# Kernel tuning notes

Hardware: AMD Instinct MI355X
Metric: run time of the kernel (lower is better)

Reference implementation:

```python
import jax, jax.numpy as jnp
import numpy as np

B, T, EMB, H = 8, 1024, 128, 8


def setup_inputs() -> dict:
    key = jax.random.key(0)
    ks = jax.random.split(key, 7)
    s = 0.02
    return {
        "x": jax.random.normal(ks[0], (B, T, EMB), dtype=jnp.float32),
        "mask": jax.random.randint(ks[1], (1, T, T), 0, 2, dtype=jnp.int32),
        "Wk": (jax.random.normal(ks[2], (EMB * H, EMB), dtype=jnp.float32) * s),
        "Wq": (jax.random.normal(ks[3], (EMB * H, EMB), dtype=jnp.float32) * s),
        "Wv": (jax.random.normal(ks[4], (EMB * H, EMB), dtype=jnp.float32) * s),
        "Wu": (jax.random.normal(ks[5], (EMB, EMB * H), dtype=jnp.float32) * s),
        "bu": (jax.random.normal(ks[6], (EMB,), dtype=jnp.float32) * s),
    }


def reference(x, mask, Wk, Wq, Wv, Wu, bu):
    b, t, e = x.shape  # e == emb; per-head dim also == emb in this module
    h = Wk.shape[0] // e
    # projections: (b,t,e) @ (e, h*e) -> (b,t,h,e) -> (b,h,t,e)
    q = (x @ Wq.T).reshape(b, t, h, e).transpose(0, 2, 1, 3)
    k = (x @ Wk.T).reshape(b, t, h, e).transpose(0, 2, 1, 3)
    v = (x @ Wv.T).reshape(b, t, h, e).transpose(0, 2, 1, 3)
    scale = e ** 0.25  # torch scales q and k each by e**(1/4)
    dot = jnp.einsum('bhqe,bhke->bhqk', q / scale, k / scale)
    # causal mask: strictly-upper triangle (offset=1) set to -inf FIRST
    causal = jnp.triu(jnp.ones((t, t), dtype=bool), k=1)
    dot = jnp.where(causal, -jnp.inf, dot)
    # padding mask: where mask==0 set to -1e9 (overwrites -inf where overlapping)
    dot = jnp.where(mask[:, None] == 0, jnp.float32(-1e9), dot)
    attn = jax.nn.softmax(dot, axis=-1)
    out = jnp.einsum('bhqk,bhke->bhqe', attn, v)
    out = out.transpose(0, 2, 1, 3).reshape(b, t, h * e)
    return out @ Wu.T + bu
```

## Files before the change

kernel.cpp:

```cpp
#include <hip/hip_runtime.h>

#define Bn 8
#define Hn 8
#define Tn 1024
#define Dn 128

typedef __attribute__((ext_vector_type(8))) short bf16x8;
typedef __attribute__((ext_vector_type(4))) float f32x4;

typedef __attribute__((address_space(3))) unsigned int lds_as_t;
typedef __attribute__((address_space(1))) const unsigned int glb_as_t;

static __device__ __forceinline__ void gload_lds16(const unsigned short* g, unsigned short* l) {
    __builtin_amdgcn_global_load_lds((glb_as_t*)g, (lds_as_t*)l, 16, 0, 0);
}
static __device__ __forceinline__ void gload_lds16b(const char* g, char* l) {
    __builtin_amdgcn_global_load_lds((glb_as_t*)g, (lds_as_t*)l, 16, 0, 0);
}

static __device__ __forceinline__ unsigned short f2bf(float f) {
    union { float f; unsigned int u; } v; v.f = f;
    unsigned int u = v.u;
    return (unsigned short)((u + 0x7FFFu + ((u >> 16) & 1u)) >> 16);
}
static __device__ __forceinline__ int pack_bf16_trunc(float lo, float hi) {
    union { float f; unsigned int u; } a, b;
    a.f = lo; b.f = hi;
    return (int)__builtin_amdgcn_perm(b.u, a.u, 0x07060302u);
}

__global__ __launch_bounds__(256, 2) void qkv_kernel(
    const float* __restrict__ x,  const float* __restrict__ Wq,
    const float* __restrict__ Wk, const float* __restrict__ Wv,
    const float* __restrict__ Wu, const int* __restrict__ mask,
    const float* __restrict__ bu, float* __restrict__ out,
    unsigned short* __restrict__ wuF, unsigned long long* __restrict__ mbits,
    char* __restrict__ Q, char* __restrict__ K, unsigned short* __restrict__ Vt)
{
    const int bx = blockIdx.x, by = blockIdx.y;
    const int tid  = threadIdx.x;
    const int wave = tid >> 6;
    const int lane = tid & 63;
    const int l16  = lane & 15;
    const int quad = lane >> 4;
    const int wm = wave & 1, wn = wave >> 1;
    const int which = by >> 3;
    const int h_ = by & 7;
    const int bid = h_ * 64 + bx;

    __shared__ __align__(16) unsigned short As[128 * 128];
    __shared__ __align__(16) unsigned short Bs[128 * 128];

    if (which == 0) {
        int base = (bid * 4 + wave) * 8;
#pragma unroll
        for (int i = 0; i < 8; i++) {
            int widx = base + i;
            int row = widx >> 4, kt = widx & 15;
            int v = mask[row * Tn + kt * 64 + lane];
            unsigned long long b = __ballot(v != 0);
            if (lane == 0) mbits[kt * Tn + row] = b;
        }
    } else if (which == 1) {
        if (tid < 32) {
            int id = bid * 32 + tid;
            int lane_ = id & 63;
            int fid = id >> 6;
            int nt = fid & 7, ks = (fid >> 3) & 3, h = fid >> 5;
            int row = nt * 16 + (lane_ & 15);
            int col = h * 128 + ks * 32 + (lane_ >> 4) * 8;
            const float* src = Wu + (size_t)row * 1024 + col;
            float4 f0 = *(const float4*)(src);
            float4 f1 = *(const float4*)(src + 4);
            unsigned short o[8];
            o[0] = f2bf(f0.x); o[1] = f2bf(f0.y); o[2] = f2bf(f0.z); o[3] = f2bf(f0.w);
            o[4] = f2bf(f1.x); o[5] = f2bf(f1.y); o[6] = f2bf(f1.z); o[7] = f2bf(f1.w);
            *(ushort4*)(wuF + (size_t)id * 8)     = *(ushort4*)&o[0];
            *(ushort4*)(wuF + (size_t)id * 8 + 4) = *(ushort4*)&o[4];
        }
    } else {
        int f4 = bid * 512 + tid * 2;
#pragma unroll
        for (int i = 0; i < 2; i++)
            ((float4*)out)[f4 + i] = ((const float4*)bu)[(f4 + i) & 31];
    }

    const float* wsel = (which == 0) ? Wq : (which == 1) ? Wk : Wv;
    const float* Asrc = x + (size_t)(bx * 128) * 128;
    const float* Bsrc = wsel + (size_t)(h_ * 128) * 128;

#pragma unroll
    for (int it = 0; it < 16; it++) {
        int idx = it * 1024 + tid * 4;
        int row = idx >> 7, col = idx & 127;
        int dst = row * 128 + ((((col >> 3) ^ (row & 15)) << 3) | (col & 7));
        float4 fa = *(const float4*)(Asrc + idx);
        ushort4 oa;
        oa.x = f2bf(fa.x); oa.y = f2bf(fa.y); oa.z = f2bf(fa.z); oa.w = f2bf(fa.w);
        *(ushort4*)(&As[dst]) = oa;
        float4 fb = *(const float4*)(Bsrc + idx);
        ushort4 ob;
        ob.x = f2bf(fb.x); ob.y = f2bf(fb.y); ob.z = f2bf(fb.z); ob.w = f2bf(fb.w);
        *(ushort4*)(&Bs[dst]) = ob;
    }
    __syncthreads();

    bf16x8 a[4][4];
#pragma unroll
    for (int mt = 0; mt < 4; mt++) {
        int row = wm * 64 + mt * 16 + l16;
#pragma unroll
        for (int ks = 0; ks < 4; ks++)
            a[mt][ks] = *(const bf16x8*)(&As[row * 128 + (((ks * 4 + quad) ^ (row & 15)) << 3)]);
    }

    f32x4 acc[4][4];
#pragma unroll
    for (int nt = 0; nt < 4; nt++) {
        int row = wn * 64 + nt * 16 + l16;
        bf16x8 b4[4];
#pragma unroll
        for (int ks = 0; ks < 4; ks++)
            b4[ks] = *(const bf16x8*)(&Bs[row * 128 + (((ks * 4 + quad) ^ (row & 15)) << 3)]);
#pragma unroll
        for (int mt = 0; mt < 4; mt++) {
            f32x4 c = {0.f, 0.f, 0.f, 0.f};
#pragma unroll
            for (int ks = 0; ks < 4; ks++)
                c = __builtin_amdgcn_mfma_f32_16x16x32_bf16(a[mt][ks], b4[ks], c, 0, 0, 0);
            acc[mt][nt] = c;
        }
    }

    const int b_ = bx >> 3;
    if (which < 2) {
        __syncthreads();
        char* escr = (char*)As;
#pragma unroll
        for (int mt = 0; mt < 4; mt++) {
#pragma unroll
            for (int nt = 0; nt < 4; nt++) {
                int w = __builtin_amdgcn_cvt_pk_fp8_f32(acc[mt][nt][0], acc[mt][nt][1], 0, false);
                w = __builtin_amdgcn_cvt_pk_fp8_f32(acc[mt][nt][2], acc[mt][nt][3], w, true);
                int col = wn * 64 + nt * 16 + l16;
#pragma unroll
                for (int r = 0; r < 4; r++)
                    escr[(wm * 64 + mt * 16 + quad * 4 + r) * 144 + col] = (char)(w >> (8 * r));
            }
        }
        __syncthreads();
        int row = tid >> 1;
        int t_in = (bx & 7) * 128 + row;
        char* dst = (which == 0) ? Q : K;
        size_t rowbase = ((size_t)((b_ * Hn + h_) * Tn + t_in)) * 128;
#pragma unroll
        for (int i = 0; i < 4; i++) {
            int c = (tid & 1) * 4 + i;
            int4 v = *(const int4*)(escr + row * 144 + c * 16);
            int cc = (which == 1) ? (c ^ (row & 7)) : c;
            *(int4*)(dst + rowbase + cc * 16) = v;
        }
    } else {
#pragma unroll
        for (int mt = 0; mt < 4; mt++) {
            int m_base = bx * 128 + wm * 64 + mt * 16 + quad * 4;
            int t0 = m_base & 1023;
#pragma unroll
            for (int nt = 0; nt < 4; nt++) {
                int e_ = wn * 64 + nt * 16 + l16;
                int kt_ = t0 >> 6, tc0 = t0 & 63;
                size_t off = ((((size_t)(b_ * Hn + h_) * 16 + kt_) * 128 + e_) << 6)
                           + ((((tc0 >> 3) ^ (e_ & 7)) << 3) | (tc0 & 7));
                ushort4 v4;
                v4.x = f2bf(acc[mt][nt][0]); v4.y = f2bf(acc[mt][nt][1]);
                v4.z = f2bf(acc[mt][nt][2]); v4.w = f2bf(acc[mt][nt][3]);
                *(ushort4*)(Vt + off) = v4;
            }
        }
    }
}

__global__ __launch_bounds__(256, 2) void attn_kernel(
    const char* __restrict__ Q,
    const char* __restrict__ K,
    const unsigned short* __restrict__ Vt,
    const unsigned long long* __restrict__ mbits,
    const unsigned short* __restrict__ wuF,
    float* __restrict__ out)
{
    const int id   = blockIdx.x;
    const int bh   = id & 63;
    const int t_   = id >> 6;
    const int qb   = (t_ < 4) ? t_ : 11 - t_;
    const int wave = threadIdx.x >> 6;
    const int lane = threadIdx.x & 63;
    const int l16  = lane & 15;
    const int quad = lane >> 4;

    __shared__ __align__(16) char kbuf[2][64 * 128];
    __shared__ __align__(16) unsigned short vbuf[2][128 * 64];

    const char* Qb = Q  + (size_t)bh * Tn * Dn;
    const char* Kb = K  + (size_t)bh * Tn * Dn;
    const unsigned short* Vb = Vt + (size_t)bh * (16 * 128 * 64);

    const int blkkt = 2 * qb + 1;
    const int q0w   = qb * 128 + wave * 32;
    const int q0s[2] = { q0w, q0w + 16 };
    const int wkmax = (q0w + 31) >> 6;

    long qf[2][4];
#pragma unroll
    for (int st = 0; st < 2; st++)
#pragma unroll
        for (int ks = 0; ks < 4; ks++)
            qf[st][ks] = *(const long*)(Qb + (size_t)(q0s[st] + l16) * 128 + ks * 32 + quad * 8);

    bf16x8 ones;
#pragma unroll
    for (int j = 0; j < 8; j++) ones[j] = (short)0x3F80;

    f32x4 o[2][8];
#pragma unroll
    for (int st = 0; st < 2; st++)
#pragma unroll
        for (int et = 0; et < 8; et++) o[st][et] = (f32x4){0.f, 0.f, 0.f, 0.f};
    f32x4 lacc[2];
    lacc[0] = (f32x4){0.f, 0.f, 0.f, 0.f};
    lacc[1] = (f32x4){0.f, 0.f, 0.f, 0.f};

    const float SL = 0.12752041570284543f;

    const int idx0 = (l16 << 2) + ((quad & 1) << 7);
    const int idx1 = idx0 + 64;
    const bool hiQ = (quad >> 1) != 0;

#pragma unroll
    for (int i = 0; i < 2; i++) {
        int base = (wave * 2 + i) * 1024;
        gload_lds16b(Kb + base + lane * 16, &kbuf[0][base]);
    }
#pragma unroll
    for (int i = 0; i < 4; i++) {
        int base = (wave * 4 + i) * 512;
        gload_lds16(Vb + base + lane * 8, &vbuf[0][base]);
    }

    for (int kt = 0; kt <= blkkt; kt++) {
        const int cur = kt & 1;
        __syncthreads();

        if (kt < blkkt) {
            const char* Kg = Kb + (kt + 1) * (64 * 128);
            const unsigned short* Vg = Vb + (kt + 1) * (128 * 64);
#pragma unroll
            for (int i = 0; i < 2; i++) {
                int base = (wave * 2 + i) * 1024;
                gload_lds16b(Kg + base + lane * 16, &kbuf[cur ^ 1][base]);
            }
#pragma unroll
            for (int i = 0; i < 4; i++) {
                int base = (wave * 4 + i) * 512;
                gload_lds16(Vg + base + lane * 8, &vbuf[cur ^ 1][base]);
            }
        }

        if (kt <= wkmax) {
            unsigned long long mw[2];
            mw[0] = mbits[kt * Tn + q0s[0] + l16];
            mw[1] = mbits[kt * Tn + q0s[1] + l16];

            f32x4 s[2][4];
#pragma unroll
            for (int nt = 0; nt < 4; nt++) {
                int row = nt * 16 + l16;
                long a4[4];
#pragma unroll
                for (int ks = 0; ks < 4; ks++) {
                    int c = ks * 2 + (quad >> 1);
                    a4[ks] = *(const long*)(&kbuf[cur][row * 128 + (((c ^ (row & 7)) << 4) | ((quad & 1) << 3))]);
                }
#pragma unroll
                for (int st = 0; st < 2; st++) {
                    f32x4 c = {0.f, 0.f, 0.f, 0.f};
#pragma unroll
                    for (int ks = 0; ks < 4; ks++)
                        c = __builtin_amdgcn_mfma_f32_16x16x32_fp8_fp8(a4[ks], qf[st][ks], c, 0, 0, 0);
                    s[st][nt] = c;
                }
            }

            const int kc0 = kt * 64;
            bf16x8 pf[2][2];
#pragma unroll
            for (int st = 0; st < 2; st++) {
                const int qglob = q0s[st] + l16;
                int w[4][2];
#pragma unroll
                for (int nt = 0; nt < 4; nt++) {
                    float pv[4];
#pragma unroll
                    for (int r = 0; r < 4; r++) {
                        int bit = nt * 16 + quad * 4 + r;
                        bool live = ((mw[st] >> bit) & 1ULL) && (kc0 + bit <= qglob);
                        pv[r] = live ? __builtin_amdgcn_exp2f(s[st][nt][r] * SL) : 0.f;
                    }
                    w[nt][0] = pack_bf16_trunc(pv[0], pv[1]);
                    w[nt][1] = pack_bf16_trunc(pv[2], pv[3]);
                }
#pragma unroll
                for (int k2 = 0; k2 < 2; k2++) {
                    union { int i[4]; bf16x8 v; } u;
#pragma unroll
                    for (int d = 0; d < 4; d++) {
                        int idx = (d < 2) ? idx0 : idx1;
                        int va = __builtin_amdgcn_ds_bpermute(idx, w[2 * k2][d & 1]);
                        int vb = __builtin_amdgcn_ds_bpermute(idx, w[2 * k2 + 1][d & 1]);
                        u.i[d] = hiQ ? vb : va;
                    }
                    pf[st][k2] = u.v;
                }
            }

#pragma unroll
            for (int st = 0; st < 2; st++)
#pragma unroll
                for (int k2 = 0; k2 < 2; k2++)
                    lacc[st] = __builtin_amdgcn_mfma_f32_16x16x32_bf16(pf[st][k2], ones, lacc[st], 0, 0, 0);

#pragma unroll
            for (int et = 0; et < 8; et++) {
                int row = et * 16 + l16;
#pragma unroll
                for (int k2 = 0; k2 < 2; k2++) {
                    bf16x8 b = *(const bf16x8*)(&vbuf[cur][row * 64 + (((k2 * 4 + quad) ^ (l16 & 7)) << 3)]);
                    o[0][et] = __builtin_amdgcn_mfma_f32_16x16x32_bf16(pf[0][k2], b, o[0][et], 0, 0, 0);
                    o[1][et] = __builtin_amdgcn_mfma_f32_16x16x32_bf16(pf[1][k2], b, o[1][et], 0, 0, 0);
                }
            }
        }
    }

    __syncthreads();
    {
        bool deg = false;
#pragma unroll
        for (int st = 0; st < 2; st++)
#pragma unroll
            for (int r = 0; r < 4; r++) deg |= (lacc[st][r] == 0.f);
        if (__ballot(deg) != 0ULL) {
            unsigned short* pb = (unsigned short*)((char*)kbuf + wave * 2304);
            unsigned short dsel[2][4];
#pragma unroll
            for (int st = 0; st < 2; st++)
#pragma unroll
                for (int r = 0; r < 4; r++)
                    dsel[st][r] = (lacc[st][r] == 0.f) ? (unsigned short)0x3F80 : (unsigned short)0;
            for (int kt = 0; kt < 16; kt++) {
#pragma unroll
                for (int st = 0; st < 2; st++) {
                    int qrow = q0s[st] + quad * 4;
                    unsigned long long mw2[4];
#pragma unroll
                    for (int r = 0; r < 4; r++) mw2[r] = mbits[kt * Tn + qrow + r];
#pragma unroll
                    for (int nt = 0; nt < 4; nt++) {
                        int bi = nt * 16 + l16;
#pragma unroll
                        for (int r = 0; r < 4; r++)
                            pb[(quad * 4 + r) * 72 + bi] = ((mw2[r] >> bi) & 1ULL) ? (unsigned short)0 : dsel[st][r];
                    }
                    bf16x8 pf[2];
#pragma unroll
                    for (int k2 = 0; k2 < 2; k2++)
                        pf[k2] = *(const bf16x8*)(&pb[l16 * 72 + k2 * 32 + quad * 8]);
#pragma unroll
                    for (int k2 = 0; k2 < 2; k2++)
                        lacc[st] = __builtin_amdgcn_mfma_f32_16x16x32_bf16(pf[k2], ones, lacc[st], 0, 0, 0);
                    const unsigned short* Vg = Vb + kt * (128 * 64);
#pragma unroll
                    for (int et = 0; et < 8; et++) {
#pragma unroll
                        for (int k2 = 0; k2 < 2; k2++) {
                            bf16x8 b = *(const bf16x8*)(Vg + (et * 16 + l16) * 64 + (((k2 * 4 + quad) ^ (l16 & 7)) << 3));
                            o[st][et] = __builtin_amdgcn_mfma_f32_16x16x32_bf16(pf[k2], b, o[st][et], 0, 0, 0);
                        }
                    }
                }
            }
        }
    }

    const int b_ = bh >> 3, h_ = bh & 7;
    const unsigned short* wf = wuF + (size_t)h_ * (4 * 8 * 64 * 8);
#pragma unroll
    for (int st = 0; st < 2; st++) {
        unsigned short* tile = (unsigned short*)((char*)vbuf + wave * 4608);
#pragma unroll
        for (int r = 0; r < 4; r++) {
            float inv = 1.f / lacc[st][r];
            int row = quad * 4 + r;
#pragma unroll
            for (int et = 0; et < 8; et++)
                tile[row * 144 + et * 16 + l16] = f2bf(o[st][et][r] * inv);
        }

        bf16x8 a4[4];
#pragma unroll
        for (int ks = 0; ks < 4; ks++)
            a4[ks] = *(const bf16x8*)(&tile[l16 * 144 + ks * 32 + quad * 8]);

        f32x4 acc2[8];
#pragma unroll
        for (int nt = 0; nt < 8; nt++) acc2[nt] = (f32x4){0.f, 0.f, 0.f, 0.f};
#pragma unroll
        for (int ks = 0; ks < 4; ks++) {
#pragma unroll
            for (int nt = 0; nt < 8; nt++) {
                bf16x8 b = *(const bf16x8*)(wf + ((size_t)(ks * 8 + nt) * 64 + lane) * 8);
                acc2[nt] = __builtin_amdgcn_mfma_f32_16x16x32_bf16(a4[ks], b, acc2[nt], 0, 0, 0);
            }
        }

#pragma unroll
        for (int nt = 0; nt < 8; nt++) {
            int n = nt * 16 + l16;
#pragma unroll
            for (int r = 0; r < 4; r++) {
                int q = q0s[st] + quad * 4 + r;
                atomicAdd(&out[(size_t)(b_ * Tn + q) * Dn + n], acc2[nt][r]);
            }
        }
    }
}

extern "C" void kernel_launch(void* const* d_in, const int* in_sizes, int n_in,
                              void* d_out, int out_size, void* d_ws, size_t ws_size,
                              hipStream_t stream) {
    const float* x   = (const float*)d_in[0];
    const int* mask  = (const int*)d_in[1];
    const float* Wk  = (const float*)d_in[2];
    const float* Wq  = (const float*)d_in[3];
    const float* Wv  = (const float*)d_in[4];
    const float* Wu  = (const float*)d_in[5];
    const float* bu  = (const float*)d_in[6];
    float* out = (float*)d_out;

    char* ws = (char*)d_ws;
    unsigned short* wuF = (unsigned short*)ws; ws += (size_t)128 * 1024 * 2;
    char* Qf  = ws; ws += (size_t)64 * 1024 * 128;
    char* Kf  = ws; ws += (size_t)64 * 1024 * 128;
    unsigned short* Vtw = (unsigned short*)ws; ws += (size_t)64 * 1024 * 128 * 2;
    unsigned long long* mb = (unsigned long long*)ws; ws += (size_t)1024 * 16 * 8;

    qkv_kernel<<<dim3(64, 24), 256, 0, stream>>>(x, Wq, Wk, Wv, Wu, mask, bu, out,
                                                 wuF, mb, Qf, Kf, Vtw);
    attn_kernel<<<dim3(512), 256, 0, stream>>>(Qf, Kf, Vtw, mb, wuF, out);
}
```

Baseline: 143.7 us.

## Shrink attention query tile to 64 rows and double the grid

The attention kernel now gives each block a 64-row query tile, one 16-row strip per wave, instead of 128 rows with two strips per wave. The grid doubles to 1024 blocks, ordered longest causal tile first, and launch bounds rise to 3 blocks per SM. Fewer accumulators per thread should allow higher occupancy and better load balance across the causal workload. In exchange, each K/V tile is reused by half as many query rows, so K/V traffic and per-tile sync overhead go up.

```diff
diff --git a/kernel.cpp b/kernel.cpp
--- a/kernel.cpp
+++ b/kernel.cpp
@@ -180,7 +180,7 @@
     }
 }
 
-__global__ __launch_bounds__(256, 2) void attn_kernel(
+__global__ __launch_bounds__(256, 3) void attn_kernel(
     const char* __restrict__ Q,
     const char* __restrict__ K,
     const unsigned short* __restrict__ Vt,
@@ -189,9 +189,8 @@
     float* __restrict__ out)
 {
     const int id   = blockIdx.x;
+    const int qt   = 15 - (id >> 6);
     const int bh   = id & 63;
-    const int t_   = id >> 6;
-    const int qb   = (t_ < 4) ? t_ : 11 - t_;
     const int wave = threadIdx.x >> 6;
     const int lane = threadIdx.x & 63;
     const int l16  = lane & 15;
@@ -204,30 +203,22 @@
     const char* Kb = K  + (size_t)bh * Tn * Dn;
     const unsigned short* Vb = Vt + (size_t)bh * (16 * 128 * 64);
 
-    const int blkkt = 2 * qb + 1;
-    const int q0w   = qb * 128 + wave * 32;
-    const int q0s[2] = { q0w, q0w + 16 };
-    const int wkmax = (q0w + 31) >> 6;
-
-    long qf[2][4];
-#pragma unroll
-    for (int st = 0; st < 2; st++)
-#pragma unroll
-        for (int ks = 0; ks < 4; ks++)
-            qf[st][ks] = *(const long*)(Qb + (size_t)(q0s[st] + l16) * 128 + ks * 32 + quad * 8);
+    const int q0 = qt * 64 + wave * 16;
+    const int qrow = q0 + quad * 4;
+
+    long qf[4];
+#pragma unroll
+    for (int ks = 0; ks < 4; ks++)
+        qf[ks] = *(const long*)(Qb + (size_t)(q0 + l16) * 128 + ks * 32 + quad * 8);
 
     bf16x8 ones;
 #pragma unroll
     for (int j = 0; j < 8; j++) ones[j] = (short)0x3F80;
 
-    f32x4 o[2][8];
-#pragma unroll
-    for (int st = 0; st < 2; st++)
-#pragma unroll
-        for (int et = 0; et < 8; et++) o[st][et] = (f32x4){0.f, 0.f, 0.f, 0.f};
-    f32x4 lacc[2];
-    lacc[0] = (f32x4){0.f, 0.f, 0.f, 0.f};
-    lacc[1] = (f32x4){0.f, 0.f, 0.f, 0.f};
+    f32x4 o[8];
+#pragma unroll
+    for (int et = 0; et < 8; et++) o[et] = (f32x4){0.f, 0.f, 0.f, 0.f};
+    f32x4 lacc = {0.f, 0.f, 0.f, 0.f};
 
     const float SL = 0.12752041570284543f;
 
@@ -246,11 +237,11 @@
         gload_lds16(Vb + base + lane * 8, &vbuf[0][base]);
     }
 
-    for (int kt = 0; kt <= blkkt; kt++) {
+    for (int kt = 0; kt <= qt; kt++) {
         const int cur = kt & 1;
         __syncthreads();
 
-        if (kt < blkkt) {
+        if (kt < qt) {
             const char* Kg = Kb + (kt + 1) * (64 * 128);
             const unsigned short* Vg = Vb + (kt + 1) * (128 * 64);
 #pragma unroll
@@ -265,126 +256,103 @@
             }
         }
 
-        if (kt <= wkmax) {
-            unsigned long long mw[2];
-            mw[0] = mbits[kt * Tn + q0s[0] + l16];
-            mw[1] = mbits[kt * Tn + q0s[1] + l16];
-
-            f32x4 s[2][4];
-#pragma unroll
-            for (int nt = 0; nt < 4; nt++) {
-                int row = nt * 16 + l16;
-                long a4[4];
-#pragma unroll
-                for (int ks = 0; ks < 4; ks++) {
-                    int c = ks * 2 + (quad >> 1);
-                    a4[ks] = *(const long*)(&kbuf[cur][row * 128 + (((c ^ (row & 7)) << 4) | ((quad & 1) << 3))]);
-                }
-#pragma unroll
-                for (int st = 0; st < 2; st++) {
-                    f32x4 c = {0.f, 0.f, 0.f, 0.f};
-#pragma unroll
-                    for (int ks = 0; ks < 4; ks++)
-                        c = __builtin_amdgcn_mfma_f32_16x16x32_fp8_fp8(a4[ks], qf[st][ks], c, 0, 0, 0);
-                    s[st][nt] = c;
-                }
-            }
-
-            const int kc0 = kt * 64;
-            bf16x8 pf[2][2];
-#pragma unroll
-            for (int st = 0; st < 2; st++) {
-                const int qglob = q0s[st] + l16;
-                int w[4][2];
-#pragma unroll
-                for (int nt = 0; nt < 4; nt++) {
-                    float pv[4];
-#pragma unroll
-                    for (int r = 0; r < 4; r++) {
-                        int bit = nt * 16 + quad * 4 + r;
-                        bool live = ((mw[st] >> bit) & 1ULL) && (kc0 + bit <= qglob);
-                        pv[r] = live ? __builtin_amdgcn_exp2f(s[st][nt][r] * SL) : 0.f;
-                    }
-                    w[nt][0] = pack_bf16_trunc(pv[0], pv[1]);
-                    w[nt][1] = pack_bf16_trunc(pv[2], pv[3]);
-                }
-#pragma unroll
-                for (int k2 = 0; k2 < 2; k2++) {
-                    union { int i[4]; bf16x8 v; } u;
-#pragma unroll
-                    for (int d = 0; d < 4; d++) {
-                        int idx = (d < 2) ? idx0 : idx1;
-                        int va = __builtin_amdgcn_ds_bpermute(idx, w[2 * k2][d & 1]);
-                        int vb = __builtin_amdgcn_ds_bpermute(idx, w[2 * k2 + 1][d & 1]);
-                        u.i[d] = hiQ ? vb : va;
-                    }
-                    pf[st][k2] = u.v;
-                }
-            }
-
-#pragma unroll
-            for (int st = 0; st < 2; st++)
-#pragma unroll
-                for (int k2 = 0; k2 < 2; k2++)
-                    lacc[st] = __builtin_amdgcn_mfma_f32_16x16x32_bf16(pf[st][k2], ones, lacc[st], 0, 0, 0);
-
-#pragma unroll
-            for (int et = 0; et < 8; et++) {
-                int row = et * 16 + l16;
-#pragma unroll
-                for (int k2 = 0; k2 < 2; k2++) {
-                    bf16x8 b = *(const bf16x8*)(&vbuf[cur][row * 64 + (((k2 * 4 + quad) ^ (l16 & 7)) << 3)]);
-                    o[0][et] = __builtin_amdgcn_mfma_f32_16x16x32_bf16(pf[0][k2], b, o[0][et], 0, 0, 0);
-                    o[1][et] = __builtin_amdgcn_mfma_f32_16x16x32_bf16(pf[1][k2], b, o[1][et], 0, 0, 0);
-                }
+        const unsigned long long mw = mbits[kt * Tn + q0 + l16];
+
+        f32x4 s[4];
+#pragma unroll
+        for (int nt = 0; nt < 4; nt++) {
+            int row = nt * 16 + l16;
+            long a4[4];
+#pragma unroll
+            for (int ks = 0; ks < 4; ks++) {
+                int c = ks * 2 + (quad >> 1);
+                a4[ks] = *(const long*)(&kbuf[cur][row * 128 + (((c ^ (row & 7)) << 4) | ((quad & 1) << 3))]);
+            }
+            f32x4 c = {0.f, 0.f, 0.f, 0.f};
+#pragma unroll
+            for (int ks = 0; ks < 4; ks++)
+                c = __builtin_amdgcn_mfma_f32_16x16x32_fp8_fp8(a4[ks], qf[ks], c, 0, 0, 0);
+            s[nt] = c;
+        }
+
+        const int kc0 = kt * 64;
+        const int qglob = q0 + l16;
+        int w[4][2];
+#pragma unroll
+        for (int nt = 0; nt < 4; nt++) {
+            float pv[4];
+#pragma unroll
+            for (int r = 0; r < 4; r++) {
+                int bit = nt * 16 + quad * 4 + r;
+                bool live = ((mw >> bit) & 1ULL) && (kc0 + bit <= qglob);
+                pv[r] = live ? __builtin_amdgcn_exp2f(s[nt][r] * SL) : 0.f;
+            }
+            w[nt][0] = pack_bf16_trunc(pv[0], pv[1]);
+            w[nt][1] = pack_bf16_trunc(pv[2], pv[3]);
+        }
+
+        bf16x8 pf[2];
+#pragma unroll
+        for (int k2 = 0; k2 < 2; k2++) {
+            union { int i[4]; bf16x8 v; } u;
+#pragma unroll
+            for (int d = 0; d < 4; d++) {
+                int idx = (d < 2) ? idx0 : idx1;
+                int va = __builtin_amdgcn_ds_bpermute(idx, w[2 * k2][d & 1]);
+                int vb = __builtin_amdgcn_ds_bpermute(idx, w[2 * k2 + 1][d & 1]);
+                u.i[d] = hiQ ? vb : va;
+            }
+            pf[k2] = u.v;
+        }
+
+#pragma unroll
+        for (int k2 = 0; k2 < 2; k2++)
+            lacc = __builtin_amdgcn_mfma_f32_16x16x32_bf16(pf[k2], ones, lacc, 0, 0, 0);
+
+#pragma unroll
+        for (int et = 0; et < 8; et++) {
+            int row = et * 16 + l16;
+#pragma unroll
+            for (int k2 = 0; k2 < 2; k2++) {
+                bf16x8 b = *(const bf16x8*)(&vbuf[cur][row * 64 + (((k2 * 4 + quad) ^ (l16 & 7)) << 3)]);
+                o[et] = __builtin_amdgcn_mfma_f32_16x16x32_bf16(pf[k2], b, o[et], 0, 0, 0);
             }
         }
     }
 
     __syncthreads();
     {
-        bool deg = false;
-#pragma unroll
-        for (int st = 0; st < 2; st++)
-#pragma unroll
-            for (int r = 0; r < 4; r++) deg |= (lacc[st][r] == 0.f);
+        bool deg = (lacc[0] == 0.f) | (lacc[1] == 0.f) | (lacc[2] == 0.f) | (lacc[3] == 0.f);
         if (__ballot(deg) != 0ULL) {
             unsigned short* pb = (unsigned short*)((char*)kbuf + wave * 2304);
-            unsigned short dsel[2][4];
-#pragma unroll
-            for (int st = 0; st < 2; st++)
-#pragma unroll
-                for (int r = 0; r < 4; r++)
-                    dsel[st][r] = (lacc[st][r] == 0.f) ? (unsigned short)0x3F80 : (unsigned short)0;
+            unsigned short dsel[4];
+#pragma unroll
+            for (int r = 0; r < 4; r++) dsel[r] = (lacc[r] == 0.f) ? (unsigned short)0x3F80 : (unsigned short)0;
             for (int kt = 0; kt < 16; kt++) {
-#pragma unroll
-                for (int st = 0; st < 2; st++) {
-                    int qrow = q0s[st] + quad * 4;
-                    unsigned long long mw2[4];
-#pragma unroll
-                    for (int r = 0; r < 4; r++) mw2[r] = mbits[kt * Tn + qrow + r];
-#pragma unroll
-                    for (int nt = 0; nt < 4; nt++) {
-                        int bi = nt * 16 + l16;
-#pragma unroll
-                        for (int r = 0; r < 4; r++)
-                            pb[(quad * 4 + r) * 72 + bi] = ((mw2[r] >> bi) & 1ULL) ? (unsigned short)0 : dsel[st][r];
-                    }
-                    bf16x8 pf[2];
-#pragma unroll
-                    for (int k2 = 0; k2 < 2; k2++)
-                        pf[k2] = *(const bf16x8*)(&pb[l16 * 72 + k2 * 32 + quad * 8]);
-#pragma unroll
-                    for (int k2 = 0; k2 < 2; k2++)
-                        lacc[st] = __builtin_amdgcn_mfma_f32_16x16x32_bf16(pf[k2], ones, lacc[st], 0, 0, 0);
-                    const unsigned short* Vg = Vb + kt * (128 * 64);
-#pragma unroll
-                    for (int et = 0; et < 8; et++) {
-#pragma unroll
-                        for (int k2 = 0; k2 < 2; k2++) {
-                            bf16x8 b = *(const bf16x8*)(Vg + (et * 16 + l16) * 64 + (((k2 * 4 + quad) ^ (l16 & 7)) << 3));
-                            o[st][et] = __builtin_amdgcn_mfma_f32_16x16x32_bf16(pf[k2], b, o[st][et], 0, 0, 0);
-                        }
+                unsigned long long mw2[4];
+#pragma unroll
+                for (int r = 0; r < 4; r++) mw2[r] = mbits[kt * Tn + qrow + r];
+#pragma unroll
+                for (int nt = 0; nt < 4; nt++) {
+                    int bi = nt * 16 + l16;
+#pragma unroll
+                    for (int r = 0; r < 4; r++)
+                        pb[(quad * 4 + r) * 72 + bi] = ((mw2[r] >> bi) & 1ULL) ? (unsigned short)0 : dsel[r];
+                }
+                bf16x8 pf[2];
+#pragma unroll
+                for (int k2 = 0; k2 < 2; k2++)
+                    pf[k2] = *(const bf16x8*)(&pb[l16 * 72 + k2 * 32 + quad * 8]);
+#pragma unroll
+                for (int k2 = 0; k2 < 2; k2++)
+                    lacc = __builtin_amdgcn_mfma_f32_16x16x32_bf16(pf[k2], ones, lacc, 0, 0, 0);
+                const unsigned short* Vg = Vb + kt * (128 * 64);
+#pragma unroll
+                for (int et = 0; et < 8; et++) {
+#pragma unroll
+                    for (int k2 = 0; k2 < 2; k2++) {
+                        bf16x8 b = *(const bf16x8*)(Vg + (et * 16 + l16) * 64 + (((k2 * 4 + quad) ^ (l16 & 7)) << 3));
+                        o[et] = __builtin_amdgcn_mfma_f32_16x16x32_bf16(pf[k2], b, o[et], 0, 0, 0);
                     }
                 }
             }
@@ -392,17 +360,15 @@
     }
 
     const int b_ = bh >> 3, h_ = bh & 7;
-    const unsigned short* wf = wuF + (size_t)h_ * (4 * 8 * 64 * 8);
-#pragma unroll
-    for (int st = 0; st < 2; st++) {
+    {
         unsigned short* tile = (unsigned short*)((char*)vbuf + wave * 4608);
 #pragma unroll
         for (int r = 0; r < 4; r++) {
-            float inv = 1.f / lacc[st][r];
+            float inv = 1.f / lacc[r];
             int row = quad * 4 + r;
 #pragma unroll
             for (int et = 0; et < 8; et++)
-                tile[row * 144 + et * 16 + l16] = f2bf(o[st][et][r] * inv);
+                tile[row * 144 + et * 16 + l16] = f2bf(o[et][r] * inv);
         }
 
         bf16x8 a4[4];
@@ -410,6 +376,7 @@
         for (int ks = 0; ks < 4; ks++)
             a4[ks] = *(const bf16x8*)(&tile[l16 * 144 + ks * 32 + quad * 8]);
 
+        const unsigned short* wf = wuF + (size_t)h_ * (4 * 8 * 64 * 8);
         f32x4 acc2[8];
 #pragma unroll
         for (int nt = 0; nt < 8; nt++) acc2[nt] = (f32x4){0.f, 0.f, 0.f, 0.f};
@@ -427,7 +394,7 @@
             int n = nt * 16 + l16;
 #pragma unroll
             for (int r = 0; r < 4; r++) {
-                int q = q0s[st] + quad * 4 + r;
+                int q = q0 + quad * 4 + r;
                 atomicAdd(&out[(size_t)(b_ * Tn + q) * Dn + n], acc2[nt][r]);
             }
         }
@@ -455,5 +422,5 @@
 
     qkv_kernel<<<dim3(64, 24), 256, 0, stream>>>(x, Wq, Wk, Wv, Wu, mask, bu, out,
                                                  wuF, mb, Qf, Kf, Vtw);
-    attn_kernel<<<dim3(512), 256, 0, stream>>>(Qf, Kf, Vtw, mb, wuF, out);
-}
+    attn_kernel<<<dim3(1024), 256, 0, stream>>>(Qf, Kf, Vtw, mb, wuF, out);
+}
```

Result: slower. 156.8 us (+9.2%).
